# Performance work log

Hardware: AMD Instinct MI355X
Metric: run time of the kernel (lower is better)

## Reference

```python
import jax, jax.numpy as jnp
import numpy as np

# Model hyperparameters (Mamba(dim=256, expand=1, d_state=16, bimamba_type='v2'))
D_MODEL = 256      # dim; expand=1 -> d_inner = D_MODEL
D_STATE = 16
DT_RANK = 16       # ceil(256/16)
D_CONV = 4
BATCH = 2
SEQ = 4096         # H*W = 64*64


def _ln(x, g, b, eps=1e-5):
    m = jnp.mean(x, axis=-1, keepdims=True)
    v = jnp.mean((x - m) ** 2, axis=-1, keepdims=True)
    return (x - m) * jax.lax.rsqrt(v + eps) * g + b


def _causal_dwconv(x, w, b):
    # x: [B, L, d], w: [d, 1, K] (depthwise), causal padding K-1 on the left
    xt = jnp.transpose(x, (0, 2, 1))  # [B, d, L]
    y = jax.lax.conv_general_dilated(
        xt, w, window_strides=(1,), padding=[(w.shape[-1] - 1, 0)],
        dimension_numbers=('NCH', 'OIH', 'NCH'), feature_group_count=xt.shape[1])
    return jnp.transpose(y + b[None, :, None], (0, 2, 1))


def _selective_scan(u, dt, Bm, Cm, A, D, z):
    # u, dt, z: [B, L, d]; Bm, Cm: [B, L, N]; A: [d, N]; D: [d]
    def step(h, inp):
        dt_t, B_t, C_t, u_t = inp            # [B,d], [B,N], [B,N], [B,d]
        h = h * jnp.exp(dt_t[:, :, None] * A) + (dt_t * u_t)[:, :, None] * B_t[:, None, :]
        y = jnp.einsum('bdn,bn->bd', h, C_t)
        return h, y

    h0 = jnp.zeros((u.shape[0], u.shape[2], A.shape[1]), u.dtype)
    xs = (jnp.transpose(dt, (1, 0, 2)), jnp.transpose(Bm, (1, 0, 2)),
          jnp.transpose(Cm, (1, 0, 2)), jnp.transpose(u, (1, 0, 2)))
    _, ys = jax.lax.scan(step, h0, xs)       # ys: [L, B, d]
    y = jnp.transpose(ys, (1, 0, 2)) + u * D
    return y * jax.nn.silu(z)                # SiLU(z) gating (done inside mamba_inner_fn)


def _mamba_dir(xin, z, conv_w, conv_b, xproj_w, dtproj_w, dtproj_b, A_log, D):
    u = jax.nn.silu(_causal_dwconv(xin, conv_w, conv_b))
    dbl = u @ xproj_w.T                       # [B, L, dt_rank + 2*N]
    dt = dbl[..., :DT_RANK]
    Bm = dbl[..., DT_RANK:DT_RANK + D_STATE]
    Cm = dbl[..., DT_RANK + D_STATE:]
    dt = jax.nn.softplus(dt @ dtproj_w.T + dtproj_b)
    return _selective_scan(u, dt, Bm, Cm, -jnp.exp(A_log), D, z)


def setup_inputs() -> dict:
    key = jax.random.key(0)
    ks = jax.random.split(key, 24)
    d, N, R, K = D_MODEL, D_STATE, DT_RANK, D_CONV
    s = 0.02
    A_log = jnp.log(jnp.tile(jnp.arange(1, N + 1, dtype=jnp.float32)[None, :], (d, 1)))
    return {
        'input': jax.random.normal(ks[0], (BATCH, SEQ, d), jnp.float32),
        'norm_g': jnp.ones((d,), jnp.float32),
        'norm_b': jnp.zeros((d,), jnp.float32),
        'in_proj_w': jax.random.normal(ks[1], (2 * d, d), jnp.float32) * s,
        # forward-direction SSM params
        'conv_w': jax.random.normal(ks[2], (d, 1, K), jnp.float32) * 0.1,
        'conv_b': jnp.zeros((d,), jnp.float32),
        'xproj_w': jax.random.normal(ks[3], (R + 2 * N, d), jnp.float32) * s,
        'dtproj_w': jax.random.normal(ks[4], (d, R), jnp.float32) * 0.1,
        'dtproj_b': jax.random.normal(ks[5], (d,), jnp.float32) * 0.1 - 4.0,
        'A_log': A_log,
        'Dp': jnp.ones((d,), jnp.float32),
        # backward-direction SSM params (bimamba v2)
        'conv_w_b': jax.random.normal(ks[6], (d, 1, K), jnp.float32) * 0.1,
        'conv_b_b': jnp.zeros((d,), jnp.float32),
        'xproj_w_b': jax.random.normal(ks[7], (R + 2 * N, d), jnp.float32) * s,
        'dtproj_w_b': jax.random.normal(ks[8], (d, R), jnp.float32) * 0.1,
        'dtproj_b_b': jax.random.normal(ks[9], (d,), jnp.float32) * 0.1 - 4.0,
        'A_log_b': A_log,
        'Dp_b': jnp.ones((d,), jnp.float32),
        # pre-out_proj norm (use_norm=True) and out projection
        'out_norm_g': jnp.ones((d,), jnp.float32),
        'out_norm_b': jnp.zeros((d,), jnp.float32),
        'out_proj_w': jax.random.normal(ks[10], (d, d), jnp.float32) * s,
        'post_norm_g': jnp.ones((d,), jnp.float32),
        'post_norm_b': jnp.zeros((d,), jnp.float32),
    }


def reference(input, norm_g, norm_b, in_proj_w,
              conv_w, conv_b, xproj_w, dtproj_w, dtproj_b, A_log, Dp,
              conv_w_b, conv_b_b, xproj_w_b, dtproj_w_b, dtproj_b_b, A_log_b, Dp_b,
              out_norm_g, out_norm_b, out_proj_w, post_norm_g, post_norm_b):
    skip = input
    x = _ln(input, norm_g, norm_b)
    xz = x @ in_proj_w.T                      # [B, L, 2d]
    xin, z = jnp.split(xz, 2, axis=-1)
    # forward direction
    y_f = _mamba_dir(xin, z, conv_w, conv_b, xproj_w, dtproj_w, dtproj_b, A_log, Dp)
    # backward direction: flip sequence, run, flip back
    y_b = _mamba_dir(xin[:, ::-1], z[:, ::-1], conv_w_b, conv_b_b, xproj_w_b,
                     dtproj_w_b, dtproj_b_b, A_log_b, Dp_b)[:, ::-1]
    y = (y_f + y_b) * 0.5                     # if_devide_out=True
    y = _ln(y, out_norm_g, out_norm_b)        # use_norm=True
    out = y @ out_proj_w.T
    out = _ln(out, post_norm_g, post_norm_b)
    return out + skip
```

## Files before the change

### kernel.cpp

```cpp
#include <hip/hip_runtime.h>
#include <math.h>

#define DM 256
#define SQ 4096
#define BT 2
#define NS 16
#define NTOK (BT*SQ)
#define NCHK 128
#define CHL (SQ/NCHK)

typedef __attribute__((ext_vector_type(8))) short short8;
typedef __attribute__((ext_vector_type(4))) float f32x4;

__device__ __forceinline__ float sigm_(float x){ return 1.f/(1.f+__expf(-x)); }
__device__ __forceinline__ float silu_(float x){ return x*sigm_(x); }
__device__ __forceinline__ float softplus_(float x){ return (x>20.f)? x : log1pf(__expf(x)); }
__device__ __forceinline__ unsigned short f2bf(float f){
  unsigned int u = __float_as_uint(f);
  unsigned int r = (u + 0x7FFFu + ((u>>16)&1u)) >> 16;
  return (unsigned short)r;
}
__device__ __forceinline__ float bf2f(unsigned short u){
  return __uint_as_float(((unsigned int)u)<<16);
}

__global__ __launch_bounds__(256) void k_prep(
    const float* __restrict__ x, const float* __restrict__ g, const float* __restrict__ nb,
    unsigned short* __restrict__ xl,
    const float* __restrict__ Win, unsigned short* __restrict__ Wbin,
    const float* __restrict__ xw_f, const float* __restrict__ xw_b,
    const float* __restrict__ dtw_f, const float* __restrict__ dtw_b,
    unsigned short* __restrict__ Wcatb,
    const float* __restrict__ Wout, unsigned short* __restrict__ Wbout)
{
  int bx = blockIdx.x;
  int tid = threadIdx.x;
  if (bx < NTOK/4){
    int tok = bx*4 + (tid>>6);
    int lane = tid & 63;
    const float* row = x + (size_t)tok*DM;
    float4 v = *(const float4*)(row + lane*4);
    float s = v.x+v.y+v.z+v.w;
    float ss = v.x*v.x+v.y*v.y+v.z*v.z+v.w*v.w;
    #pragma unroll
    for (int o=32;o>0;o>>=1){ s += __shfl_xor(s,o,64); ss += __shfl_xor(ss,o,64); }
    float m = s*(1.f/DM);
    float r = rsqrtf(ss*(1.f/DM)-m*m+1e-5f);
    float4 gv = *(const float4*)(g + lane*4);
    float4 bv = *(const float4*)(nb + lane*4);
    ushort4 o4;
    o4.x = f2bf((v.x-m)*r*gv.x+bv.x);
    o4.y = f2bf((v.y-m)*r*gv.y+bv.y);
    o4.z = f2bf((v.z-m)*r*gv.z+bv.z);
    o4.w = f2bf((v.w-m)*r*gv.w+bv.w);
    *(ushort4*)(xl + (size_t)tok*DM + lane*4) = o4;
  } else if (bx < NTOK/4 + 128){
    int i = ((bx - NTOK/4)*256 + tid)*4;
    float4 v = *(const float4*)(Win + i);
    ushort4 o4; o4.x=f2bf(v.x); o4.y=f2bf(v.y); o4.z=f2bf(v.z); o4.w=f2bf(v.w);
    *(ushort4*)(Wbin + i) = o4;
  } else if (bx < NTOK/4 + 136){
    int idx = bx - (NTOK/4 + 128);
    int dir = idx >> 2;
    int kc = (idx & 3)*64;
    const float* xw  = dir? xw_b : xw_f;
    const float* dtw = dir? dtw_b : dtw_f;
    int d = tid;
    float dw[16];
    #pragma unroll
    for (int r=0;r<16;r++) dw[r] = dtw[d*16+r];
    unsigned short* Wd = Wcatb + (size_t)dir*320*DM + (size_t)d*DM + kc;
    for (int kk=0;kk<64;kk++){
      float acc = 0.f;
      #pragma unroll
      for (int r=0;r<16;r++) acc += dw[r]*xw[r*DM + kc + kk];
      Wd[kk] = f2bf(acc);
    }
    if (d < 64){
      unsigned short* Wr = Wcatb + (size_t)dir*320*DM + (size_t)(256+d)*DM + kc;
      if (d < 32){
        const float* src = xw + (size_t)(16+d)*DM + kc;
        for (int kk=0;kk<64;kk++) Wr[kk] = f2bf(src[kk]);
      } else {
        for (int kk=0;kk<64;kk++) Wr[kk] = 0;
      }
    }
  } else {
    int i = ((bx - (NTOK/4 + 136))*256 + tid)*4;
    float4 v = *(const float4*)(Wout + i);
    ushort4 o4; o4.x=f2bf(v.x); o4.y=f2bf(v.y); o4.z=f2bf(v.z); o4.w=f2bf(v.w);
    *(ushort4*)(Wbout + i) = o4;
  }
}

__global__ __launch_bounds__(256) void k_inproj_mfma(
    const unsigned short* __restrict__ xl, const unsigned short* __restrict__ Wb,
    float* __restrict__ xin, unsigned short* __restrict__ zb)
{
  int tid = threadIdx.x;
  int wid = tid >> 6, lane = tid & 63;
  int wm = wid >> 1, wn = wid & 1;
  int row0 = blockIdx.x*128 + wm*64;
  int col0 = blockIdx.y*64 + wn*32;
  int lr = lane & 15;
  int lg = lane >> 4;
  f32x4 acc[4][2];
  #pragma unroll
  for (int m=0;m<4;m++)
    #pragma unroll
    for (int n=0;n<2;n++) acc[m][n] = (f32x4){0.f,0.f,0.f,0.f};

  #pragma unroll
  for (int k0=0;k0<DM;k0+=32){
    short8 a[4], b[2];
    #pragma unroll
    for (int m=0;m<4;m++)
      a[m] = *(const short8*)(xl + (size_t)(row0 + m*16 + lr)*DM + k0 + lg*8);
    #pragma unroll
    for (int n=0;n<2;n++)
      b[n] = *(const short8*)(Wb + (size_t)(col0 + n*16 + lr)*DM + k0 + lg*8);
    #pragma unroll
    for (int m=0;m<4;m++)
      #pragma unroll
      for (int n=0;n<2;n++)
        acc[m][n] = __builtin_amdgcn_mfma_f32_16x16x32_bf16(a[m], b[n], acc[m][n], 0,0,0);
  }
  if (blockIdx.y < 4){
    #pragma unroll
    for (int m=0;m<4;m++)
      #pragma unroll
      for (int n=0;n<2;n++)
        #pragma unroll
        for (int r=0;r<4;r++){
          int rr = row0 + m*16 + lg*4 + r;
          int cc = col0 + n*16 + lr;
          xin[(size_t)rr*DM + cc] = acc[m][n][r];
        }
  } else {
    int cb = col0 - 256;
    #pragma unroll
    for (int m=0;m<4;m++)
      #pragma unroll
      for (int n=0;n<2;n++)
        #pragma unroll
        for (int r=0;r<4;r++){
          int rr = row0 + m*16 + lg*4 + r;
          int cc = cb + n*16 + lr;
          zb[(size_t)rr*DM + cc] = f2bf(acc[m][n][r]);
        }
  }
}

__global__ __launch_bounds__(256) void k_conv2(
    const float* __restrict__ xin,
    const float* __restrict__ cw_f, const float* __restrict__ cb_f,
    const float* __restrict__ cw_b, const float* __restrict__ cb_b,
    unsigned short* __restrict__ ufb, unsigned short* __restrict__ ubb)
{
  int d = threadIdx.x;
  int b = blockIdx.y;
  int t0 = blockIdx.x*16;
  float wf0=cw_f[d*4], wf1=cw_f[d*4+1], wf2=cw_f[d*4+2], wf3=cw_f[d*4+3];
  float wb0=cw_b[d*4], wb1=cw_b[d*4+1], wb2=cw_b[d*4+2], wb3=cw_b[d*4+3];
  float bfv = cb_f[d], bbv = cb_b[d];
  const float* xbase = xin + (size_t)b*SQ*DM + d;
  float r0 = (t0-3>=0)? xbase[(size_t)(t0-3)*DM] : 0.f;
  float r1 = (t0-2>=0)? xbase[(size_t)(t0-2)*DM] : 0.f;
  float r2 = (t0-1>=0)? xbase[(size_t)(t0-1)*DM] : 0.f;
  float r3 = xbase[(size_t)(t0+0)*DM];
  float r4 = xbase[(size_t)(t0+1)*DM];
  float r5 = xbase[(size_t)(t0+2)*DM];
  float r6 = xbase[(size_t)(t0+3)*DM];
  for (int i=0;i<16;i++){
    int t = t0+i;
    float vf = silu_(bfv + wf0*r0 + wf1*r1 + wf2*r2 + wf3*r3);
    ufb[((size_t)b*SQ+t)*DM + d] = f2bf(vf);
    float vb = silu_(bbv + wb3*r3 + wb2*r4 + wb1*r5 + wb0*r6);
    ubb[((size_t)b*SQ+(SQ-1-t))*DM + d] = f2bf(vb);
    r0=r1; r1=r2; r2=r3; r3=r4; r4=r5; r5=r6;
    int tn = t+4;
    r6 = (tn<=SQ-1)? xbase[(size_t)tn*DM] : 0.f;
  }
}

__global__ __launch_bounds__(256) void k_xproj_mfma(
    const unsigned short* __restrict__ ufb, const unsigned short* __restrict__ ubb,
    const unsigned short* __restrict__ Wcatb,
    const float* __restrict__ dtbias_f, const float* __restrict__ dtbias_b,
    unsigned short* __restrict__ dt16f, unsigned short* __restrict__ dt16b,
    float* __restrict__ bmf, float* __restrict__ cmf,
    float* __restrict__ bmb, float* __restrict__ cmb)
{
  int dir = blockIdx.z;
  const unsigned short* u  = dir? ubb : ufb;
  const unsigned short* Wc = Wcatb + (size_t)dir*320*DM;
  const float* dbi = dir? dtbias_b : dtbias_f;
  unsigned short* dt = dir? dt16b : dt16f;
  float* bm = dir? bmb : bmf;
  float* cm = dir? cmb : cmf;
  int tid = threadIdx.x;
  int wid = tid >> 6, lane = tid & 63;
  int wm = wid >> 1, wn = wid & 1;
  int row0 = blockIdx.x*128 + wm*64;
  int col0 = blockIdx.y*64 + wn*32;
  int lr = lane & 15, lg = lane >> 4;
  f32x4 acc[4][2];
  #pragma unroll
  for (int m=0;m<4;m++)
    #pragma unroll
    for (int n=0;n<2;n++) acc[m][n] = (f32x4){0.f,0.f,0.f,0.f};
  #pragma unroll
  for (int k0=0;k0<DM;k0+=32){
    short8 a[4], b[2];
    #pragma unroll
    for (int m=0;m<4;m++)
      a[m] = *(const short8*)(u + (size_t)(row0 + m*16 + lr)*DM + k0 + lg*8);
    #pragma unroll
    for (int n=0;n<2;n++)
      b[n] = *(const short8*)(Wc + (size_t)(col0 + n*16 + lr)*DM + k0 + lg*8);
    #pragma unroll
    for (int m=0;m<4;m++)
      #pragma unroll
      for (int n=0;n<2;n++)
        acc[m][n] = __builtin_amdgcn_mfma_f32_16x16x32_bf16(a[m], b[n], acc[m][n], 0,0,0);
  }
  if (blockIdx.y < 4){
    #pragma unroll
    for (int n=0;n<2;n++){
      int cc = col0 + n*16 + lr;
      float bias = dbi[cc];
      #pragma unroll
      for (int m=0;m<4;m++)
        #pragma unroll
        for (int r=0;r<4;r++){
          int rr = row0 + m*16 + lg*4 + r;
          dt[(size_t)rr*DM + cc] = f2bf(softplus_(acc[m][n][r] + bias));
        }
    }
  } else if (wn == 0){
    #pragma unroll
    for (int n=0;n<2;n++){
      float* outp = n ? cm : bm;
      #pragma unroll
      for (int m=0;m<4;m++)
        #pragma unroll
        for (int r=0;r<4;r++){
          int rr = row0 + m*16 + lg*4 + r;
          outp[(size_t)rr*NS + lr] = acc[m][n][r];
        }
    }
  }
}

__global__ __launch_bounds__(256) void k_scan1(
    const unsigned short* __restrict__ dtf, const unsigned short* __restrict__ dtb,
    const unsigned short* __restrict__ ufb, const unsigned short* __restrict__ ubb,
    const float* __restrict__ bmf, const float* __restrict__ bmb,
    const float* __restrict__ alog_f, const float* __restrict__ alog_b,
    float* __restrict__ apf, float* __restrict__ hsf,
    float* __restrict__ apb, float* __restrict__ hsb)
{
  int c = blockIdx.x, b = blockIdx.y, dir = blockIdx.z;
  const unsigned short* dt = dir? dtb : dtf;
  const unsigned short* u  = dir? ubb : ufb;
  const float* bmp= dir? bmb : bmf;
  const float* al = dir? alog_b : alog_f;
  float* ap = dir? apb : apf;
  float* hs = dir? hsb : hsf;
  int d = threadIdx.x;
  __shared__ float sB[CHL*NS];
  for (int i=threadIdx.x;i<CHL*NS;i+=256) sB[i] = bmp[((size_t)b*SQ + c*CHL)*NS + i];
  float A[NS];
  #pragma unroll
  for (int n=0;n<NS;n++) A[n] = -__expf(al[d*NS+n]);
  float h[NS] = {};
  float dts = 0.f;
  __syncthreads();
  for (int t=0;t<CHL;t++){
    size_t idx = ((size_t)b*SQ + c*CHL + t)*DM + d;
    float dtv = bf2f(dt[idx]);
    float uv  = bf2f(u[idx]);
    float du  = dtv*uv;
    dts += dtv;
    #pragma unroll
    for (int n=0;n<NS;n++) h[n] = h[n]*__expf(dtv*A[n]) + du*sB[t*NS+n];
  }
  size_t o = (((size_t)b*NCHK + c)*DM + d)*NS;
  #pragma unroll
  for (int n=0;n<NS;n++){ hs[o+n] = h[n]; ap[o+n] = __expf(A[n]*dts); }
}

__global__ __launch_bounds__(256) void k_scan2(
    float* __restrict__ apf, float* __restrict__ hsf,
    float* __restrict__ apb, float* __restrict__ hsb)
{
  __shared__ float sa[NCHK][64];
  __shared__ float sv[NCHK][64];
  __shared__ float segA[4][64], segV[4][64];
  int bx = blockIdx.x;
  int dg = bx & 63, b = (bx>>6)&1, dir = bx>>7;
  const float* ap = dir? apb : apf;
  float* hs = dir? hsb : hsf;
  int dn = threadIdx.x & 63;
  int cg = threadIdx.x >> 6;
  size_t base = (size_t)b*NCHK*4096 + dg*64 + dn;
  for (int i=0;i<32;i++){
    int c = cg*32 + i;
    size_t idx = base + (size_t)c*4096;
    sa[c][dn] = ap[idx];
    sv[c][dn] = hs[idx];
  }
  __syncthreads();
  float A = 1.f, V = 0.f;
  for (int i=0;i<32;i++){
    int c = cg*32 + i;
    float a = sa[c][dn], v = sv[c][dn];
    V = a*V + v;
    A = A*a;
  }
  segA[cg][dn] = A; segV[cg][dn] = V;
  __syncthreads();
  float pre = 0.f;
  for (int s=0;s<cg;s++) pre = segA[s][dn]*pre + segV[s][dn];
  float xv = pre;
  for (int i=0;i<32;i++){
    int c = cg*32 + i;
    size_t idx = base + (size_t)c*4096;
    hs[idx] = xv;
    float a = sa[c][dn], v = sv[c][dn];
    xv = a*xv + v;
  }
}

__global__ __launch_bounds__(256) void k_scan3(
    const unsigned short* __restrict__ dtf, const unsigned short* __restrict__ dtb,
    const unsigned short* __restrict__ ufb, const unsigned short* __restrict__ ubb,
    const float* __restrict__ bmf, const float* __restrict__ bmb,
    const float* __restrict__ cmf, const float* __restrict__ cmb,
    const float* __restrict__ alf, const float* __restrict__ alb,
    const float* __restrict__ Df, const float* __restrict__ Db,
    const unsigned short* __restrict__ zb,
    const float* __restrict__ hsf, const float* __restrict__ hsb,
    unsigned short* __restrict__ yf, unsigned short* __restrict__ yb)
{
  int c = blockIdx.x, b = blockIdx.y;
  int dir = blockIdx.z;
  const unsigned short* dt = dir? dtb : dtf;
  const unsigned short* u  = dir? ubb : ufb;
  const float* bmp= dir? bmb : bmf;
  const float* cmp= dir? cmb : cmf;
  const float* al = dir? alb : alf;
  const float* Dv = dir? Db  : Df;
  const float* hs = dir? hsb : hsf;
  unsigned short* yout = dir? yb : yf;
  int d = threadIdx.x;
  __shared__ float sB[CHL*NS];
  __shared__ float sC[CHL*NS];
  for (int i=threadIdx.x;i<CHL*NS;i+=256){
    sB[i] = bmp[((size_t)b*SQ + c*CHL)*NS + i];
    sC[i] = cmp[((size_t)b*SQ + c*CHL)*NS + i];
  }
  float A[NS], h[NS];
  size_t o = (((size_t)b*NCHK + c)*DM + d)*NS;
  #pragma unroll
  for (int n=0;n<NS;n++){ A[n] = -__expf(al[d*NS+n]); h[n] = hs[o+n]; }
  float Dd = Dv[d];
  __syncthreads();
  for (int t=0;t<CHL;t++){
    int gt = c*CHL + t;
    size_t idx = ((size_t)b*SQ + gt)*DM + d;
    float dtv = bf2f(dt[idx]);
    float uv  = bf2f(u[idx]);
    float du  = dtv*uv;
    float y = 0.f;
    #pragma unroll
    for (int n=0;n<NS;n++){
      h[n] = h[n]*__expf(dtv*A[n]) + du*sB[t*NS+n];
      y += h[n]*sC[t*NS+n];
    }
    y += uv*Dd;
    int torig = dir ? (SQ-1-gt) : gt;
    size_t oidx = ((size_t)b*SQ + torig)*DM + d;
    float zv = bf2f(zb[oidx]);
    yout[oidx] = f2bf(y * (zv * sigm_(zv)));
  }
}

__global__ __launch_bounds__(256) void k_ycvt(const unsigned short* __restrict__ yf,
                                              const unsigned short* __restrict__ yb,
                                              const float* __restrict__ og, const float* __restrict__ ob,
                                              unsigned short* __restrict__ ybf){
  int tok = blockIdx.x*4 + (threadIdx.x>>6);
  int lane = threadIdx.x & 63;
  size_t base = (size_t)tok*DM;
  ushort4 hf = *(const ushort4*)(yf + base + lane*4);
  ushort4 hb = *(const ushort4*)(yb + base + lane*4);
  float4 v;
  v.x = 0.5f*(bf2f(hf.x)+bf2f(hb.x));
  v.y = 0.5f*(bf2f(hf.y)+bf2f(hb.y));
  v.z = 0.5f*(bf2f(hf.z)+bf2f(hb.z));
  v.w = 0.5f*(bf2f(hf.w)+bf2f(hb.w));
  float s = v.x+v.y+v.z+v.w;
  float ss = v.x*v.x+v.y*v.y+v.z*v.z+v.w*v.w;
  #pragma unroll
  for (int o=32;o>0;o>>=1){ s += __shfl_xor(s,o,64); ss += __shfl_xor(ss,o,64); }
  float m = s*(1.f/DM);
  float r = rsqrtf(ss*(1.f/DM)-m*m+1e-5f);
  float4 gv = *(const float4*)(og + lane*4);
  float4 bv = *(const float4*)(ob + lane*4);
  ushort4 o4;
  o4.x = f2bf((v.x-m)*r*gv.x+bv.x);
  o4.y = f2bf((v.y-m)*r*gv.y+bv.y);
  o4.z = f2bf((v.z-m)*r*gv.z+bv.z);
  o4.w = f2bf((v.w-m)*r*gv.w+bv.w);
  *(ushort4*)(ybf + base + lane*4) = o4;
}

#define SOS 266
__global__ __launch_bounds__(256) void k_final_mfma(
    const unsigned short* __restrict__ ybf, const unsigned short* __restrict__ Wb,
    const float* __restrict__ pg, const float* __restrict__ pb,
    const float* __restrict__ skip, float* __restrict__ out)
{
  __shared__ float sOut[32*SOS];
  __shared__ float sm[32], sr[32];
  int tid = threadIdx.x;
  int wid = tid >> 6, lane = tid & 63;
  int lr = lane & 15, lg = lane >> 4;
  int row0 = blockIdx.x*32;
  int col0 = wid*64;
  f32x4 acc[2][4];
  #pragma unroll
  for (int m=0;m<2;m++)
    #pragma unroll
    for (int n=0;n<4;n++) acc[m][n] = (f32x4){0.f,0.f,0.f,0.f};
  #pragma unroll
  for (int k0=0;k0<DM;k0+=32){
    short8 a[2], b[4];
    #pragma unroll
    for (int m=0;m<2;m++)
      a[m] = *(const short8*)(ybf + (size_t)(row0 + m*16 + lr)*DM + k0 + lg*8);
    #pragma unroll
    for (int n=0;n<4;n++)
      b[n] = *(const short8*)(Wb + (size_t)(col0 + n*16 + lr)*DM + k0 + lg*8);
    #pragma unroll
    for (int m=0;m<2;m++)
      #pragma unroll
      for (int n=0;n<4;n++)
        acc[m][n] = __builtin_amdgcn_mfma_f32_16x16x32_bf16(a[m], b[n], acc[m][n], 0,0,0);
  }
  #pragma unroll
  for (int m=0;m<2;m++)
    #pragma unroll
    for (int n=0;n<4;n++)
      #pragma unroll
      for (int r=0;r<4;r++)
        sOut[(m*16 + lg*4 + r)*SOS + col0 + n*16 + lr] = acc[m][n][r];
  __syncthreads();
  for (int j=0;j<8;j++){
    int rrow = wid*8 + j;
    const float* rp = &sOut[rrow*SOS + lane*4];
    float2 v0 = *(const float2*)(rp);
    float2 v1 = *(const float2*)(rp+2);
    float s = v0.x+v0.y+v1.x+v1.y;
    float ss = v0.x*v0.x+v0.y*v0.y+v1.x*v1.x+v1.y*v1.y;
    #pragma unroll
    for (int o=32;o>0;o>>=1){ s += __shfl_xor(s,o,64); ss += __shfl_xor(ss,o,64); }
    if (lane==0){ float m=s*(1.f/DM); sm[rrow]=m; sr[rrow]=rsqrtf(ss*(1.f/DM)-m*m+1e-5f); }
  }
  __syncthreads();
  float gv = pg[tid], bv = pb[tid];
  for (int rrow=0;rrow<32;rrow++){
    int tok = row0 + rrow;
    float v = (sOut[rrow*SOS + tid]-sm[rrow])*sr[rrow]*gv + bv + skip[(size_t)tok*DM + tid];
    out[(size_t)tok*DM + tid] = v;
  }
}

extern "C" void kernel_launch(void* const* d_in, const int* in_sizes, int n_in,
                              void* d_out, int out_size, void* d_ws, size_t ws_size,
                              hipStream_t stream)
{
  const float* input      = (const float*)d_in[0];
  const float* norm_g     = (const float*)d_in[1];
  const float* norm_b     = (const float*)d_in[2];
  const float* in_proj_w  = (const float*)d_in[3];
  const float* conv_w     = (const float*)d_in[4];
  const float* conv_b     = (const float*)d_in[5];
  const float* xproj_w    = (const float*)d_in[6];
  const float* dtproj_w   = (const float*)d_in[7];
  const float* dtproj_b   = (const float*)d_in[8];
  const float* A_log      = (const float*)d_in[9];
  const float* Dp         = (const float*)d_in[10];
  const float* conv_w_b   = (const float*)d_in[11];
  const float* conv_b_b   = (const float*)d_in[12];
  const float* xproj_w_b  = (const float*)d_in[13];
  const float* dtproj_w_b = (const float*)d_in[14];
  const float* dtproj_b_b = (const float*)d_in[15];
  const float* A_log_b    = (const float*)d_in[16];
  const float* Dp_b       = (const float*)d_in[17];
  const float* out_norm_g = (const float*)d_in[18];
  const float* out_norm_b = (const float*)d_in[19];
  const float* out_proj_w = (const float*)d_in[20];
  const float* post_norm_g= (const float*)d_in[21];
  const float* post_norm_b= (const float*)d_in[22];
  float* out = (float*)d_out;

  float* ws = (float*)d_ws;
  const size_t M2 = (size_t)NTOK*DM;
  const size_t SCH = (size_t)BT*NCHK*DM*NS;
  float* xin = ws;
  unsigned short* y16f = (unsigned short*)ws;
  unsigned short* y16b = (unsigned short*)ws + M2;
  unsigned short* zbuf = (unsigned short*)(ws + M2);
  unsigned short* auxw = (unsigned short*)(ws + M2 + M2/2);
  unsigned short* Wbin  = auxw;
  unsigned short* Wcatb = auxw + 131072;
  unsigned short* Wbout = auxw + 131072 + 163840;
  unsigned short* dt16f = (unsigned short*)(ws + 3*M2);
  unsigned short* dt16b = dt16f + M2;
  unsigned short* ufb = (unsigned short*)(ws + 4*M2);
  unsigned short* ubb = ufb + M2;
  float* p   = ws + 5*M2;
  float* bmf = p;              p += (size_t)NTOK*NS;
  float* cmf = p;              p += (size_t)NTOK*NS;
  float* bmb = p;              p += (size_t)NTOK*NS;
  float* cmb = p;              p += (size_t)NTOK*NS;
  float* apf = p;              p += SCH;
  float* hsf = p;              p += SCH;
  float* apb = p;              p += SCH;
  float* hsb = p;              p += SCH;
  unsigned short* xlbf = (unsigned short*)apf;
  unsigned short* ybf  = (unsigned short*)apf;

  k_prep<<<NTOK/4 + 136 + 64, 256, 0, stream>>>(input, norm_g, norm_b, xlbf,
                                                in_proj_w, Wbin,
                                                xproj_w, xproj_w_b, dtproj_w, dtproj_w_b, Wcatb,
                                                out_proj_w, Wbout);
  k_inproj_mfma<<<dim3(NTOK/128, 8, 1), 256, 0, stream>>>(xlbf, Wbin, xin, zbuf);
  k_conv2<<<dim3(SQ/16, BT), 256, 0, stream>>>(xin, conv_w, conv_b, conv_w_b, conv_b_b,
                                               ufb, ubb);
  k_xproj_mfma<<<dim3(NTOK/128, 5, 2), 256, 0, stream>>>(ufb, ubb, Wcatb,
                                                         dtproj_b, dtproj_b_b,
                                                         dt16f, dt16b, bmf, cmf, bmb, cmb);
  k_scan1<<<dim3(NCHK, BT, 2), 256, 0, stream>>>(dt16f, dt16b, ufb, ubb, bmf, bmb,
                                                 A_log, A_log_b, apf, hsf, apb, hsb);
  k_scan2<<<256, 256, 0, stream>>>(apf, hsf, apb, hsb);
  k_scan3<<<dim3(NCHK, BT, 2), 256, 0, stream>>>(dt16f, dt16b, ufb, ubb, bmf, bmb, cmf, cmb,
                                                 A_log, A_log_b, Dp, Dp_b, zbuf, hsf, hsb,
                                                 y16f, y16b);
  k_ycvt<<<NTOK/4, 256, 0, stream>>>(y16f, y16b, out_norm_g, out_norm_b, ybf);
  k_final_mfma<<<NTOK/32, 256, 0, stream>>>(ybf, Wbout, post_norm_g, post_norm_b, input, out);
}
```

Before: 144.6 us.

## Fuse depthwise conv into in-proj GEMM and out-norm into final GEMM

Folds the causal depthwise conv and SiLU into the in-projection kernel. The x-half tile is kept in shared memory and the 3-row halo on each side is recomputed with a scalar dot product, so the fp32 xin buffer never goes to global memory. Separately, the average-plus-LayerNorm kernel is merged into the final out-projection GEMM, which normalizes 32 rows into LDS before the MFMA loop. This removes two launches and two global round trips, at the cost of redundant halo GEMM work and larger shared-memory use per block.

New measurement: 144.4 us. Within noise of the previous version (-0.1%).

```diff
diff --git a/kernel.cpp b/kernel.cpp
--- a/kernel.cpp
+++ b/kernel.cpp
@@ -93,17 +93,21 @@
   }
 }
 
-__global__ __launch_bounds__(256) void k_inproj_mfma(
+__global__ __launch_bounds__(256) void k_inproj_conv(
     const unsigned short* __restrict__ xl, const unsigned short* __restrict__ Wb,
-    float* __restrict__ xin, unsigned short* __restrict__ zb)
-{
+    const float* __restrict__ cw_f, const float* __restrict__ cb_f,
+    const float* __restrict__ cw_b, const float* __restrict__ cb_b,
+    unsigned short* __restrict__ ufb, unsigned short* __restrict__ ubb,
+    unsigned short* __restrict__ zb)
+{
+  __shared__ float xs[134][68];
+  __shared__ unsigned short xh[6][256];
   int tid = threadIdx.x;
   int wid = tid >> 6, lane = tid & 63;
   int wm = wid >> 1, wn = wid & 1;
   int row0 = blockIdx.x*128 + wm*64;
   int col0 = blockIdx.y*64 + wn*32;
-  int lr = lane & 15;
-  int lg = lane >> 4;
+  int lr = lane & 15, lg = lane >> 4;
   f32x4 acc[4][2];
   #pragma unroll
   for (int m=0;m<4;m++)
@@ -125,18 +129,7 @@
       for (int n=0;n<2;n++)
         acc[m][n] = __builtin_amdgcn_mfma_f32_16x16x32_bf16(a[m], b[n], acc[m][n], 0,0,0);
   }
-  if (blockIdx.y < 4){
-    #pragma unroll
-    for (int m=0;m<4;m++)
-      #pragma unroll
-      for (int n=0;n<2;n++)
-        #pragma unroll
-        for (int r=0;r<4;r++){
-          int rr = row0 + m*16 + lg*4 + r;
-          int cc = col0 + n*16 + lr;
-          xin[(size_t)rr*DM + cc] = acc[m][n][r];
-        }
-  } else {
+  if (blockIdx.y >= 4){
     int cb = col0 - 256;
     #pragma unroll
     for (int m=0;m<4;m++)
@@ -148,38 +141,52 @@
           int cc = cb + n*16 + lr;
           zb[(size_t)rr*DM + cc] = f2bf(acc[m][n][r]);
         }
-  }
-}
-
-__global__ __launch_bounds__(256) void k_conv2(
-    const float* __restrict__ xin,
-    const float* __restrict__ cw_f, const float* __restrict__ cb_f,
-    const float* __restrict__ cw_b, const float* __restrict__ cb_b,
-    unsigned short* __restrict__ ufb, unsigned short* __restrict__ ubb)
-{
-  int d = threadIdx.x;
-  int b = blockIdx.y;
-  int t0 = blockIdx.x*16;
-  float wf0=cw_f[d*4], wf1=cw_f[d*4+1], wf2=cw_f[d*4+2], wf3=cw_f[d*4+3];
-  float wb0=cw_b[d*4], wb1=cw_b[d*4+1], wb2=cw_b[d*4+2], wb3=cw_b[d*4+3];
-  float bfv = cb_f[d], bbv = cb_b[d];
-  const float* xbase = xin + (size_t)b*SQ*DM + d;
-  float r0 = (t0-3>=0)? xbase[(size_t)(t0-3)*DM] : 0.f;
-  float r1 = (t0-2>=0)? xbase[(size_t)(t0-2)*DM] : 0.f;
-  float r2 = (t0-1>=0)? xbase[(size_t)(t0-1)*DM] : 0.f;
-  float r3 = xbase[(size_t)(t0+0)*DM];
-  float r4 = xbase[(size_t)(t0+1)*DM];
-  float r5 = xbase[(size_t)(t0+2)*DM];
-  float r6 = xbase[(size_t)(t0+3)*DM];
-  for (int i=0;i<16;i++){
-    int t = t0+i;
-    float vf = silu_(bfv + wf0*r0 + wf1*r1 + wf2*r2 + wf3*r3);
-    ufb[((size_t)b*SQ+t)*DM + d] = f2bf(vf);
-    float vb = silu_(bbv + wb3*r3 + wb2*r4 + wb1*r5 + wb0*r6);
-    ubb[((size_t)b*SQ+(SQ-1-t))*DM + d] = f2bf(vb);
-    r0=r1; r1=r2; r2=r3; r3=r4; r4=r5; r5=r6;
-    int tn = t+4;
-    r6 = (tn<=SQ-1)? xbase[(size_t)tn*DM] : 0.f;
+    return;
+  }
+  #pragma unroll
+  for (int m=0;m<4;m++)
+    #pragma unroll
+    for (int n=0;n<2;n++)
+      #pragma unroll
+      for (int r=0;r<4;r++)
+        xs[wm*64 + m*16 + lg*4 + r + 3][wn*32 + n*16 + lr] = acc[m][n][r];
+  int b_  = blockIdx.x >> 5;
+  int lt0 = (blockIdx.x & 31)*128;
+  for (int i=tid; i<6*256; i+=256){
+    int hr = i >> 8, k = i & 255;
+    int lt = (hr<3)? (lt0-3+hr) : (lt0+128+(hr-3));
+    unsigned short v = 0;
+    if (lt >= 0 && lt < SQ) v = xl[((size_t)b_*SQ+lt)*DM + k];
+    xh[hr][k] = v;
+  }
+  __syncthreads();
+  for (int i=tid; i<384; i+=256){
+    int hr = i >> 6, col = i & 63;
+    int gcol = blockIdx.y*64 + col;
+    float acch = 0.f;
+    for (int k=0;k<256;k+=8){
+      short8 xa = *(const short8*)&xh[hr][k];
+      short8 wv = *(const short8*)(Wb + (size_t)gcol*DM + k);
+      #pragma unroll
+      for (int e=0;e<8;e++) acch += bf2f((unsigned short)xa[e])*bf2f((unsigned short)wv[e]);
+    }
+    int xr = (hr<3)? hr : (131 + hr - 3);
+    xs[xr][col] = acch;
+  }
+  __syncthreads();
+  int col = tid & 63, tg = tid >> 6;
+  int gd = blockIdx.y*64 + col;
+  float wf0=cw_f[gd*4], wf1=cw_f[gd*4+1], wf2=cw_f[gd*4+2], wf3=cw_f[gd*4+3];
+  float wb0=cw_b[gd*4], wb1=cw_b[gd*4+1], wb2=cw_b[gd*4+2], wb3=cw_b[gd*4+3];
+  float bfv = cb_f[gd], bbv = cb_b[gd];
+  for (int i=0;i<32;i++){
+    int r = tg*32 + i;
+    float x0=xs[r][col], x1=xs[r+1][col], x2=xs[r+2][col], x3=xs[r+3][col];
+    float vf = silu_(bfv + wf0*x0 + wf1*x1 + wf2*x2 + wf3*x3);
+    ufb[((size_t)b_*SQ + lt0 + r)*DM + gd] = f2bf(vf);
+    float x4=xs[r+4][col], x5=xs[r+5][col], x6=xs[r+6][col];
+    float vb = silu_(bbv + wb3*x3 + wb2*x4 + wb1*x5 + wb0*x6);
+    ubb[((size_t)b_*SQ + (SQ-1-(lt0+r)))*DM + gd] = f2bf(vb);
   }
 }
 
@@ -386,48 +393,47 @@
   }
 }
 
-__global__ __launch_bounds__(256) void k_ycvt(const unsigned short* __restrict__ yf,
-                                              const unsigned short* __restrict__ yb,
-                                              const float* __restrict__ og, const float* __restrict__ ob,
-                                              unsigned short* __restrict__ ybf){
-  int tok = blockIdx.x*4 + (threadIdx.x>>6);
-  int lane = threadIdx.x & 63;
-  size_t base = (size_t)tok*DM;
-  ushort4 hf = *(const ushort4*)(yf + base + lane*4);
-  ushort4 hb = *(const ushort4*)(yb + base + lane*4);
-  float4 v;
-  v.x = 0.5f*(bf2f(hf.x)+bf2f(hb.x));
-  v.y = 0.5f*(bf2f(hf.y)+bf2f(hb.y));
-  v.z = 0.5f*(bf2f(hf.z)+bf2f(hb.z));
-  v.w = 0.5f*(bf2f(hf.w)+bf2f(hb.w));
-  float s = v.x+v.y+v.z+v.w;
-  float ss = v.x*v.x+v.y*v.y+v.z*v.z+v.w*v.w;
-  #pragma unroll
-  for (int o=32;o>0;o>>=1){ s += __shfl_xor(s,o,64); ss += __shfl_xor(ss,o,64); }
-  float m = s*(1.f/DM);
-  float r = rsqrtf(ss*(1.f/DM)-m*m+1e-5f);
-  float4 gv = *(const float4*)(og + lane*4);
-  float4 bv = *(const float4*)(ob + lane*4);
-  ushort4 o4;
-  o4.x = f2bf((v.x-m)*r*gv.x+bv.x);
-  o4.y = f2bf((v.y-m)*r*gv.y+bv.y);
-  o4.z = f2bf((v.z-m)*r*gv.z+bv.z);
-  o4.w = f2bf((v.w-m)*r*gv.w+bv.w);
-  *(ushort4*)(ybf + base + lane*4) = o4;
-}
-
 #define SOS 266
-__global__ __launch_bounds__(256) void k_final_mfma(
-    const unsigned short* __restrict__ ybf, const unsigned short* __restrict__ Wb,
+__global__ __launch_bounds__(256) void k_final2(
+    const unsigned short* __restrict__ y16f, const unsigned short* __restrict__ y16b,
+    const float* __restrict__ og, const float* __restrict__ ob,
+    const unsigned short* __restrict__ Wb,
     const float* __restrict__ pg, const float* __restrict__ pb,
     const float* __restrict__ skip, float* __restrict__ out)
 {
+  __shared__ unsigned short yn[32][272];
   __shared__ float sOut[32*SOS];
   __shared__ float sm[32], sr[32];
   int tid = threadIdx.x;
   int wid = tid >> 6, lane = tid & 63;
+  int row0 = blockIdx.x*32;
+  for (int j=0;j<8;j++){
+    int rrow = wid*8 + j;
+    size_t base = (size_t)(row0+rrow)*DM + lane*4;
+    ushort4 hf = *(const ushort4*)(y16f + base);
+    ushort4 hb = *(const ushort4*)(y16b + base);
+    float4 v;
+    v.x = 0.5f*(bf2f(hf.x)+bf2f(hb.x));
+    v.y = 0.5f*(bf2f(hf.y)+bf2f(hb.y));
+    v.z = 0.5f*(bf2f(hf.z)+bf2f(hb.z));
+    v.w = 0.5f*(bf2f(hf.w)+bf2f(hb.w));
+    float s = v.x+v.y+v.z+v.w;
+    float ss = v.x*v.x+v.y*v.y+v.z*v.z+v.w*v.w;
+    #pragma unroll
+    for (int o=32;o>0;o>>=1){ s += __shfl_xor(s,o,64); ss += __shfl_xor(ss,o,64); }
+    float m = s*(1.f/DM);
+    float r = rsqrtf(ss*(1.f/DM)-m*m+1e-5f);
+    float4 gv = *(const float4*)(og + lane*4);
+    float4 bv = *(const float4*)(ob + lane*4);
+    ushort4 o4;
+    o4.x = f2bf((v.x-m)*r*gv.x+bv.x);
+    o4.y = f2bf((v.y-m)*r*gv.y+bv.y);
+    o4.z = f2bf((v.z-m)*r*gv.z+bv.z);
+    o4.w = f2bf((v.w-m)*r*gv.w+bv.w);
+    *(ushort4*)&yn[rrow][lane*4] = o4;
+  }
+  __syncthreads();
   int lr = lane & 15, lg = lane >> 4;
-  int row0 = blockIdx.x*32;
   int col0 = wid*64;
   f32x4 acc[2][4];
   #pragma unroll
@@ -439,7 +445,7 @@
     short8 a[2], b[4];
     #pragma unroll
     for (int m=0;m<2;m++)
-      a[m] = *(const short8*)(ybf + (size_t)(row0 + m*16 + lr)*DM + k0 + lg*8);
+      a[m] = *(const short8*)&yn[m*16 + lr][k0 + lg*8];
     #pragma unroll
     for (int n=0;n<4;n++)
       b[n] = *(const short8*)(Wb + (size_t)(col0 + n*16 + lr)*DM + k0 + lg*8);
@@ -509,7 +515,6 @@
   float* ws = (float*)d_ws;
   const size_t M2 = (size_t)NTOK*DM;
   const size_t SCH = (size_t)BT*NCHK*DM*NS;
-  float* xin = ws;
   unsigned short* y16f = (unsigned short*)ws;
   unsigned short* y16b = (unsigned short*)ws + M2;
   unsigned short* zbuf = (unsigned short*)(ws + M2);
@@ -531,15 +536,14 @@
   float* apb = p;              p += SCH;
   float* hsb = p;              p += SCH;
   unsigned short* xlbf = (unsigned short*)apf;
-  unsigned short* ybf  = (unsigned short*)apf;
 
   k_prep<<<NTOK/4 + 136 + 64, 256, 0, stream>>>(input, norm_g, norm_b, xlbf,
                                                 in_proj_w, Wbin,
                                                 xproj_w, xproj_w_b, dtproj_w, dtproj_w_b, Wcatb,
                                                 out_proj_w, Wbout);
-  k_inproj_mfma<<<dim3(NTOK/128, 8, 1), 256, 0, stream>>>(xlbf, Wbin, xin, zbuf);
-  k_conv2<<<dim3(SQ/16, BT), 256, 0, stream>>>(xin, conv_w, conv_b, conv_w_b, conv_b_b,
-                                               ufb, ubb);
+  k_inproj_conv<<<dim3(NTOK/128, 8, 1), 256, 0, stream>>>(xlbf, Wbin,
+                                                          conv_w, conv_b, conv_w_b, conv_b_b,
+                                                          ufb, ubb, zbuf);
   k_xproj_mfma<<<dim3(NTOK/128, 5, 2), 256, 0, stream>>>(ufb, ubb, Wcatb,
                                                          dtproj_b, dtproj_b_b,
                                                          dt16f, dt16b, bmf, cmf, bmb, cmb);
@@ -549,6 +553,6 @@
   k_scan3<<<dim3(NCHK, BT, 2), 256, 0, stream>>>(dt16f, dt16b, ufb, ubb, bmf, bmb, cmf, cmb,
                                                  A_log, A_log_b, Dp, Dp_b, zbuf, hsf, hsb,
                                                  y16f, y16b);
-  k_ycvt<<<NTOK/4, 256, 0, stream>>>(y16f, y16b, out_norm_g, out_norm_b, ybf);
-  k_final_mfma<<<NTOK/32, 256, 0, stream>>>(ybf, Wbout, post_norm_g, post_norm_b, input, out);
-}
+  k_final2<<<NTOK/32, 256, 0, stream>>>(y16f, y16b, out_norm_g, out_norm_b, Wbout,
+                                        post_norm_g, post_norm_b, input, out);
+}
```
